# Kernel optimization log

Hardware: AMD Instinct MI355X
Metric: run time of the kernel (lower is better)

The kernel has to match this reference:

```python
import jax, jax.numpy as jnp
import numpy as np
import math

B, S, HID, H, WBAND = 2, 4096, 768, 12, 128
D = HID // H  # 64


def _band_qk(q, k, w):
    """q,k: [B,S,H,D] -> banded scores [B,S,H,2w+1] (offset d -> key pos i+d-w)."""
    b, s, h, d = q.shape
    nc = s // w
    kp = jnp.pad(k, ((0, 0), (w, w), (0, 0), (0, 0)))  # zero padding_value
    idx = (jnp.arange(nc) * w)[:, None] + jnp.arange(3 * w)[None, :]  # [nc,3w]
    kw = kp[:, idx]                                   # [B,nc,3w,H,D]
    qc = q.reshape(b, nc, w, h, d)
    scores = jnp.einsum('bcxhd,bcyhd->bchxy', qc, kw)  # [B,nc,H,w,3w]
    # extract diagonals: P[x,dd] = scores[x, x+dd] via flatten/skew trick
    flat = scores.reshape(b, nc, h, w * 3 * w)
    flat = jnp.pad(flat, ((0, 0), (0, 0), (0, 0), (0, w)))
    diag = flat.reshape(b, nc, h, w, 3 * w + 1)[..., : 2 * w + 1]
    return diag.transpose(0, 1, 3, 2, 4).reshape(b, s, h, 2 * w + 1)


def _band_pv(p, v, w):
    """p: [B,S,H,2w+1], v: [B,S,H,D] -> context [B,S,H,D]."""
    b, s, h, k = p.shape
    d = v.shape[-1]
    nc = s // w
    vp = jnp.pad(v, ((0, 0), (w, w), (0, 0), (0, 0)))
    idx = (jnp.arange(nc) * w)[:, None] + jnp.arange(3 * w)[None, :]
    vw = vp[:, idx]                                   # [B,nc,3w,H,D]
    pc = p.reshape(b, nc, w, h, k).transpose(0, 1, 3, 2, 4)  # [B,nc,H,w,2w+1]
    pc = jnp.pad(pc, ((0, 0), (0, 0), (0, 0), (0, 0), (0, w)))  # [..,w,3w+1]
    band = pc.reshape(b, nc, h, w * (3 * w + 1))[..., : w * 3 * w]
    band = band.reshape(b, nc, h, w, 3 * w)           # M[x, x+dd] = p[x,dd]
    ctx = jnp.einsum('bchxy,bcyhd->bcxhd', band, vw)  # [B,nc,w,H,D]
    return ctx.reshape(b, s, h, d)


def setup_inputs() -> dict:
    key = jax.random.key(0)
    ks = jax.random.split(key, 8)
    init = lambda k, shp: (jax.random.normal(k, shp, jnp.float32) * 0.02)
    return {
        'x': jax.random.normal(ks[0], (B, S, HID), jnp.float32),
        'Wq': init(ks[1], (HID, HID)), 'bq': jnp.zeros((HID,), jnp.float32),
        'Wk': init(ks[2], (HID, HID)), 'bk': jnp.zeros((HID,), jnp.float32),
        'Wv': init(ks[3], (HID, HID)), 'bv': jnp.zeros((HID,), jnp.float32),
        'Wd': init(ks[4], (H, D, HID)), 'bd': jnp.zeros((HID,), jnp.float32),
        'gamma': jnp.ones((HID,), jnp.float32),
        'beta': jnp.zeros((HID,), jnp.float32),
    }


def reference(x, Wq, bq, Wk, bk, Wv, bv, Wd, bd, gamma, beta):
    w = WBAND
    b, s, _ = x.shape
    q = (x @ Wq + bq).reshape(b, s, H, D) / math.sqrt(D)
    k = (x @ Wk + bk).reshape(b, s, H, D)
    v = (x @ Wv + bv).reshape(b, s, H, D)
    scores = _band_qk(q, k, w)                        # [B,S,H,2w+1]
    # mask_invalid_locations: key pos i + d - w must lie in [0, S)
    pos = jnp.arange(s)[:, None] + jnp.arange(2 * w + 1)[None, :] - w
    valid = (pos >= 0) & (pos < s)                    # [S,2w+1]
    scores = jnp.where(valid[None, :, None, :], scores, -1e9)
    probs = jax.nn.softmax(scores, axis=-1)           # float32 softmax
    ctx = _band_pv(probs, v, w)                       # [B,S,H,D]
    proj = jnp.einsum('bfnd,ndh->bfh', ctx, Wd) + bd  # output projection
    y = x + proj                                      # residual (dropout=0)
    mu = jnp.mean(y, axis=-1, keepdims=True)
    var = jnp.mean(jnp.square(y - mu), axis=-1, keepdims=True)
    out = (y - mu) / jnp.sqrt(var + 1e-12) * gamma + beta
    return out
```

## Files before the change

### kernel.cpp

```cpp
#include <hip/hip_runtime.h>
#include <math.h>

typedef unsigned short u16;
typedef __bf16 bf16x8 __attribute__((ext_vector_type(8)));
typedef float f32x4 __attribute__((ext_vector_type(4)));

constexpr int Bc   = 2;
constexpr int Sc   = 4096;
constexpr int HIDc = 768;
constexpr int Hc   = 12;
constexpr int Dc   = 64;
constexpr int Wc   = 128;
constexpr int Mc   = Bc * Sc;

constexpr int QT3  = 128;
constexpr int NCT3 = 18;

#define VM_BAR(N) asm volatile("s_waitcnt vmcnt(" #N ")\n\ts_barrier" ::: "memory")
#define BAR()     asm volatile("s_barrier" ::: "memory")

static __device__ __forceinline__ void load_lds16(const void* g, void* l) {
    __builtin_amdgcn_global_load_lds(
        (const __attribute__((address_space(1))) void*)g,
        (__attribute__((address_space(3))) void*)l, 16, 0, 0);
}
static __device__ __forceinline__ u16 to_bf16(float f) {
    return __builtin_bit_cast(u16, (__bf16)f);
}

__global__ __launch_bounds__(256) void prep_all(
    const float* __restrict__ x, u16* __restrict__ xb, u16* __restrict__ zpad,
    const float* __restrict__ Wq, const float* __restrict__ Wk,
    const float* __restrict__ Wv, const float* __restrict__ Wd,
    u16* __restrict__ wqt, u16* __restrict__ wkt,
    u16* __restrict__ wvt, u16* __restrict__ wdt)
{
    const int bid = blockIdx.x;
    if (bid < 6144) {
        int i = bid * 256 + threadIdx.x;
        float4 v = ((const float4*)x)[i];
        ushort4 o;
        o.x = to_bf16(v.x); o.y = to_bf16(v.y);
        o.z = to_bf16(v.z); o.w = to_bf16(v.w);
        ((ushort4*)xb)[i] = o;
        if (bid == 0 && threadIdx.x < 128)
            ((int4*)zpad)[threadIdx.x] = make_int4(0, 0, 0, 0);
    } else {
        int r = bid - 6144;
        int z = r / 576, xy = r - z * 576;
        const float* W = z == 0 ? Wq : z == 1 ? Wk : z == 2 ? Wv : Wd;
        u16* T         = z == 0 ? wqt : z == 1 ? wkt : z == 2 ? wvt : wdt;
        __shared__ float t[32][33];
        const int bx = (xy % 24) * 32, by = (xy / 24) * 32;
        const int tx = threadIdx.x & 31, ty = threadIdx.x >> 5;
#pragma unroll
        for (int i = 0; i < 32; i += 8)
            t[ty + i][tx] = W[(size_t)(by + ty + i) * HIDc + bx + tx];
        __syncthreads();
#pragma unroll
        for (int i = 0; i < 32; i += 8)
            T[(size_t)(bx + ty + i) * HIDc + by + tx] = to_bf16(t[tx][ty + i]);
    }
}

__device__ __forceinline__ void stage64(const u16* __restrict__ A,
                                        const u16* __restrict__ Bt,
                                        int m0, int n0, int k0,
                                        u16* As, u16* Bs, int soff)
{
#pragma unroll
    for (int i = 0; i < 4; ++i) {
        int off  = soff + i * 1024;
        int row  = off >> 7;
        int slot = (off >> 4) & 7;
        int seg  = slot ^ (row & 7);
        load_lds16(A  + (size_t)(m0 + row) * HIDc + k0 + seg * 8, (char*)As + off);
        load_lds16(Bt + (size_t)(n0 + row) * HIDc + k0 + seg * 8, (char*)Bs + off);
    }
}

template <int SWAP>
__device__ __forceinline__ void gemm128_core(
    const u16* __restrict__ A, const u16* __restrict__ Bt,
    int m0, int n0, u16* As, u16* Bs, f32x4 (&acc)[4][4])
{
    const int lane = threadIdx.x & 63, wid = threadIdx.x >> 6;
    const int c16 = lane & 15, g = lane >> 4;
    const int wm = (wid >> 1) * 64, wn = (wid & 1) * 64;
    const int soff = wid * 4096 + lane * 16;

    stage64(A, Bt, m0, n0, 0, As, Bs, soff);
    int cur = 0;
    for (int t = 0; t < 12; ++t) {
        if (t < 11) {
            stage64(A, Bt, m0, n0, (t + 1) * 64,
                    As + (cur ^ 1) * 8192, Bs + (cur ^ 1) * 8192, soff);
            VM_BAR(8);
        } else {
            VM_BAR(0);
        }
        const u16* Ab = As + cur * 8192;
        const u16* Bb = Bs + cur * 8192;
#pragma unroll
        for (int kk = 0; kk < 2; ++kk) {
            bf16x8 af[4], bfr[4];
#pragma unroll
            for (int tt = 0; tt < 4; ++tt) {
                int ar = wm + tt * 16 + c16;
                int a8 = (kk * 4 + g) ^ (ar & 7);
                af[tt] = *(const bf16x8*)(Ab + ar * 64 + a8 * 8);
                int br = wn + tt * 16 + c16;
                int b8 = (kk * 4 + g) ^ (br & 7);
                bfr[tt] = *(const bf16x8*)(Bb + br * 64 + b8 * 8);
            }
            __builtin_amdgcn_s_setprio(1);
#pragma unroll
            for (int mt = 0; mt < 4; ++mt)
#pragma unroll
                for (int nt = 0; nt < 4; ++nt)
                    acc[mt][nt] = SWAP
                        ? __builtin_amdgcn_mfma_f32_16x16x32_bf16(
                              bfr[nt], af[mt], acc[mt][nt], 0, 0, 0)
                        : __builtin_amdgcn_mfma_f32_16x16x32_bf16(
                              af[mt], bfr[nt], acc[mt][nt], 0, 0, 0);
            __builtin_amdgcn_s_setprio(0);
        }
        BAR();
        cur ^= 1;
    }
}

__global__ __launch_bounds__(256) void gemm_qkv_mfma(
    const u16* __restrict__ xb,
    const u16* __restrict__ wqt, const u16* __restrict__ wkt,
    const u16* __restrict__ wvt,
    const float* __restrict__ bq, const float* __restrict__ bk,
    const float* __restrict__ bv,
    u16* __restrict__ qg, u16* __restrict__ kg, u16* __restrict__ vtg)
{
    __shared__ u16 As[16384], Bs[16384];
    const int z = blockIdx.z;
    const u16* Bt     = z == 0 ? wqt : z == 1 ? wkt : wvt;
    const float* bias = z == 0 ? bq : z == 1 ? bk : bv;

    const int m0 = blockIdx.x * 128, n0 = blockIdx.y * 128;
    f32x4 acc[4][4];
#pragma unroll
    for (int i = 0; i < 4; ++i)
#pragma unroll
        for (int j = 0; j < 4; ++j) acc[i][j] = (f32x4){0.f, 0.f, 0.f, 0.f};

    const int lane = threadIdx.x & 63, wid = threadIdx.x >> 6;
    const int c16 = lane & 15, g = lane >> 4;
    const int wm = (wid >> 1) * 64, wn = (wid & 1) * 64;

    if (z == 2) {
        gemm128_core<0>(xb, Bt, m0, n0, As, Bs, acc);
#pragma unroll
        for (int nt = 0; nt < 4; ++nt) {
            int n = n0 + wn + nt * 16 + c16;
            int h = n >> 6, d = n & 63;
            float bn = bias[n];
#pragma unroll
            for (int mt = 0; mt < 4; ++mt) {
                int m = m0 + wm + mt * 16 + g * 4;
                int b = m >> 12, s = m & (Sc - 1);
                size_t base = ((size_t)(b * Hc + h)) * Sc * Dc + (size_t)d * Sc + s;
                ushort4 pk;
                pk.x = to_bf16(acc[mt][nt][0] + bn);
                pk.y = to_bf16(acc[mt][nt][1] + bn);
                pk.z = to_bf16(acc[mt][nt][2] + bn);
                pk.w = to_bf16(acc[mt][nt][3] + bn);
                *(ushort4*)&vtg[base] = pk;
            }
        }
    } else {
        gemm128_core<1>(xb, Bt, m0, n0, As, Bs, acc);
        const float scale = z ? 1.0f : 0.125f;
        u16* outp = z ? kg : qg;
#pragma unroll
        for (int mt = 0; mt < 4; ++mt) {
            int m = m0 + wm + mt * 16 + c16;
            int b = m >> 12, s = m & (Sc - 1);
            size_t rowbase = (size_t)(b * Hc) * Sc * Dc + (size_t)s * Dc;
#pragma unroll
            for (int nt = 0; nt < 4; ++nt) {
                int nb = n0 + wn + nt * 16 + g * 4;
                int h = nb >> 6, d0 = nb & 63;
                float4 b4 = *(const float4*)&bias[nb];
                ushort4 pk;
                pk.x = to_bf16((acc[mt][nt][0] + b4.x) * scale);
                pk.y = to_bf16((acc[mt][nt][1] + b4.y) * scale);
                pk.z = to_bf16((acc[mt][nt][2] + b4.z) * scale);
                pk.w = to_bf16((acc[mt][nt][3] + b4.w) * scale);
                *(ushort4*)&outp[rowbase + (size_t)h * Sc * Dc + d0] = pk;
            }
        }
    }
}

__global__ __launch_bounds__(256) void gemm_proj_mfma(
    const u16* __restrict__ ctxb, const u16* __restrict__ wdt,
    const float* __restrict__ bd, const float* __restrict__ x,
    float* __restrict__ y)
{
    __shared__ u16 As[16384], Bs[16384];
    const int m0 = blockIdx.x * 128, n0 = blockIdx.y * 128;
    f32x4 acc[4][4];
#pragma unroll
    for (int i = 0; i < 4; ++i)
#pragma unroll
        for (int j = 0; j < 4; ++j) acc[i][j] = (f32x4){0.f, 0.f, 0.f, 0.f};

    gemm128_core<1>(ctxb, wdt, m0, n0, As, Bs, acc);

    const int lane = threadIdx.x & 63, wid = threadIdx.x >> 6;
    const int c16 = lane & 15, g = lane >> 4;
    const int wm = (wid >> 1) * 64, wn = (wid & 1) * 64;

#pragma unroll
    for (int mt = 0; mt < 4; ++mt) {
        int m = m0 + wm + mt * 16 + c16;
#pragma unroll
        for (int nt = 0; nt < 4; ++nt) {
            int nb = n0 + wn + nt * 16 + g * 4;
            float4 b4 = *(const float4*)&bd[nb];
            float4 x4 = *(const float4*)&x[(size_t)m * HIDc + nb];
            float4 o4;
            o4.x = acc[mt][nt][0] + b4.x + x4.x;
            o4.y = acc[mt][nt][1] + b4.y + x4.y;
            o4.z = acc[mt][nt][2] + b4.z + x4.z;
            o4.w = acc[mt][nt][3] + b4.w + x4.w;
            *(float4*)&y[(size_t)m * HIDc + nb] = o4;
        }
    }
}

__global__ __launch_bounds__(512) void band_attn_mfma(
    const u16* __restrict__ qg, const u16* __restrict__ kg,
    const u16* __restrict__ vtg, const u16* __restrict__ zpad,
    u16* __restrict__ ctxb)
{
    extern __shared__ u16 sm[];
    u16* kwin = sm;
    u16* vt   = sm + 24576;
    u16* pm   = sm;

    const int L = blockIdx.x;
    const int xcd = L & 7, tt = L >> 3;
    const int hb = xcd * 3 + (tt % 3);
    const int qc = tt / 3;
    const int h = hb % Hc, b = hb / Hc;

    const int s0 = qc * QT3;
    const int tid = threadIdx.x;
    const int lane = tid & 63, w = tid >> 6;
    const int c16 = lane & 15, g = lane >> 4;
    const size_t hbase = ((size_t)(b * Hc + h)) * Sc * Dc;

    const u16* qp = &qg[hbase + (size_t)(s0 + w * 16 + c16) * Dc + g * 8];
    bf16x8 qa0 = *(const bf16x8*)qp;
    bf16x8 qa1 = *(const bf16x8*)(qp + 32);

#pragma unroll
    for (int i = 0; i < 6; ++i) {
        int c   = i * 8 + w;
        int row = c * 8 + (lane >> 3);
        int seg = (lane & 7) ^ (lane >> 3);
        int pos = s0 - Wc + row;
        const u16* src = (pos >= 0 && pos < Sc)
                       ? &kg[hbase + (size_t)pos * Dc + seg * 8] : zpad;
        load_lds16(src, (char*)kwin + c * 1024 + (lane & 63) * 16);
    }
#pragma unroll
    for (int i = 0; i < 6; ++i) {
        int c   = i * 8 + w;
        int idx = c * 64 + lane;
        int d   = idx / 48;
        int p   = idx - d * 48;
        int seg = (p & ~7) | ((p ^ d) & 7);
        int pos0 = s0 - Wc + seg * 8;
        const u16* src = (pos0 >= 0 && pos0 < Sc)
                       ? &vtg[hbase + (size_t)d * Sc + pos0] : zpad;
        load_lds16(src, (char*)vt + idx * 16);
    }

    VM_BAR(6);

    const int tb  = w & ~1;
    const int off = (w & 1) * 16;
    f32x4 acc[NCT3];
#pragma unroll
    for (int ct = 0; ct < NCT3; ++ct) acc[ct] = (f32x4){0.f, 0.f, 0.f, 0.f};
    __builtin_amdgcn_s_setprio(1);
#pragma unroll
    for (int ct = 0; ct < NCT3; ++ct) {
        int row = (tb + ct) * 16 + c16;
        const u16* kb = kwin + row * 64;
        bf16x8 kb0 = *(const bf16x8*)(kb + (g       ^ (row & 7)) * 8);
        bf16x8 kb1 = *(const bf16x8*)(kb + ((g + 4) ^ (row & 7)) * 8);
        acc[ct] = __builtin_amdgcn_mfma_f32_16x16x32_bf16(qa0, kb0, acc[ct], 0, 0, 0);
        acc[ct] = __builtin_amdgcn_mfma_f32_16x16x32_bf16(qa1, kb1, acc[ct], 0, 0, 0);
    }
    __builtin_amdgcn_s_setprio(0);

    float mrow[4] = {-3e38f, -3e38f, -3e38f, -3e38f};
#pragma unroll
    for (int ct = 0; ct < NCT3; ++ct) {
#pragma unroll
        for (int r = 0; r < 4; ++r) {
            int ql  = g * 4 + r;
            int jl  = ct * 16 + c16 - off;
            int pos = s0 - Wc + (tb + ct) * 16 + c16;
            bool valid = (jl >= ql) && (jl <= ql + 2 * Wc) && (pos >= 0) && (pos < Sc);
            float v = valid ? acc[ct][r] : -3e38f;
            acc[ct][r] = v;
            mrow[r] = fmaxf(mrow[r], v);
        }
    }
#pragma unroll
    for (int r = 0; r < 4; ++r)
#pragma unroll
        for (int o2 = 1; o2 < 16; o2 <<= 1)
            mrow[r] = fmaxf(mrow[r], __shfl_xor(mrow[r], o2));

    float srow[4] = {0.f, 0.f, 0.f, 0.f};
#pragma unroll
    for (int ct = 0; ct < NCT3; ++ct)
#pragma unroll
        for (int r = 0; r < 4; ++r) {
            float e = __expf(acc[ct][r] - mrow[r]);
            acc[ct][r] = e;
            srow[r] += e;
        }
#pragma unroll
    for (int r = 0; r < 4; ++r)
#pragma unroll
        for (int o2 = 1; o2 < 16; o2 <<= 1)
            srow[r] += __shfl_xor(srow[r], o2);

    VM_BAR(0);

    float sq0 = __shfl(srow[0], (c16 >> 2) << 4);
    float sq1 = __shfl(srow[1], (c16 >> 2) << 4);
    float sq2 = __shfl(srow[2], (c16 >> 2) << 4);
    float sq3 = __shfl(srow[3], (c16 >> 2) << 4);
    int rr = c16 & 3;
    float sq = rr == 0 ? sq0 : rr == 1 ? sq1 : rr == 2 ? sq2 : sq3;
    float invq = 1.f / sq;

    const int qrow = w * 16 + c16;
    f32x4 o[4];
#pragma unroll
    for (int dt = 0; dt < 4; ++dt) o[dt] = (f32x4){0.f, 0.f, 0.f, 0.f};

#pragma unroll
    for (int ct = 0; ct < 10; ++ct)
#pragma unroll
        for (int r = 0; r < 4; ++r) {
            int q   = w * 16 + g * 4 + r;
            int col = ct * 16 + c16;
            int sl  = col >> 3;
            int ph  = (sl & ~7) | ((sl ^ q ^ (q >> 3)) & 7);
            pm[q * 192 + ph * 8 + (col & 7)] = to_bf16(acc[ct][r]);
        }
    __builtin_amdgcn_s_setprio(1);
#pragma unroll
    for (int ks = 0; ks < 5; ++ks) {
        int sl = ks * 4 + g;
        int ph = (sl & ~7) | ((sl ^ qrow ^ (qrow >> 3)) & 7);
        bf16x8 pa = *(const bf16x8*)(pm + qrow * 192 + ph * 8);
#pragma unroll
        for (int dt = 0; dt < 4; ++dt) {
            int d  = dt * 16 + c16;
            int vs = tb * 2 + ks * 4 + g;
            int pv = (vs & ~7) | ((vs ^ d) & 7);
            bf16x8 vb = *(const bf16x8*)(vt + d * 384 + pv * 8);
            o[dt] = __builtin_amdgcn_mfma_f32_16x16x32_bf16(vb, pa, o[dt], 0, 0, 0);
        }
    }
    __builtin_amdgcn_s_setprio(0);

#pragma unroll
    for (int ct = 10; ct < NCT3; ++ct)
#pragma unroll
        for (int r = 0; r < 4; ++r) {
            int q   = w * 16 + g * 4 + r;
            int col = ct * 16 + c16 - 160;
            int sl  = col >> 3;
            int ph  = (sl & ~7) | ((sl ^ q ^ (q >> 3)) & 7);
            pm[q * 192 + ph * 8 + (col & 7)] = to_bf16(acc[ct][r]);
        }
    __builtin_amdgcn_s_setprio(1);
#pragma unroll
    for (int ks = 0; ks < 4; ++ks) {
        int sl = ks * 4 + g;
        int ph = (sl & ~7) | ((sl ^ qrow ^ (qrow >> 3)) & 7);
        bf16x8 pa = *(const bf16x8*)(pm + qrow * 192 + ph * 8);
#pragma unroll
        for (int dt = 0; dt < 4; ++dt) {
            int d  = dt * 16 + c16;
            int vs = tb * 2 + 20 + ks * 4 + g;
            int pv = (vs & ~7) | ((vs ^ d) & 7);
            bf16x8 vb = *(const bf16x8*)(vt + d * 384 + pv * 8);
            o[dt] = __builtin_amdgcn_mfma_f32_16x16x32_bf16(vb, pa, o[dt], 0, 0, 0);
        }
    }
    __builtin_amdgcn_s_setprio(0);

    const size_t crow = ((size_t)(b * Sc + s0 + qrow)) * HIDc + h * Dc;
#pragma unroll
    for (int dt = 0; dt < 4; ++dt) {
        ushort4 pk;
        pk.x = to_bf16(o[dt][0] * invq);
        pk.y = to_bf16(o[dt][1] * invq);
        pk.z = to_bf16(o[dt][2] * invq);
        pk.w = to_bf16(o[dt][3] * invq);
        *(ushort4*)&ctxb[crow + dt * 16 + g * 4] = pk;
    }
}

__global__ __launch_bounds__(256) void ln_kernel(
    const float* __restrict__ y,
    const float* __restrict__ gamma, const float* __restrict__ beta,
    float* __restrict__ out)
{
    const int m = blockIdx.x;
    const float* row = y + (size_t)m * HIDc;
    const int t = threadIdx.x;
    float v0 = row[t], v1 = row[t + 256], v2 = row[t + 512];
    float s = v0 + v1 + v2;
    __shared__ float red[4];
    const int lane = t & 63, wid = t >> 6;
#pragma unroll
    for (int o = 1; o < 64; o <<= 1) s += __shfl_xor(s, o);
    if (lane == 0) red[wid] = s;
    __syncthreads();
    const float mu = (red[0] + red[1] + red[2] + red[3]) * (1.f / HIDc);
    v0 -= mu; v1 -= mu; v2 -= mu;
    float s2 = v0 * v0 + v1 * v1 + v2 * v2;
#pragma unroll
    for (int o = 1; o < 64; o <<= 1) s2 += __shfl_xor(s2, o);
    __syncthreads();
    if (lane == 0) red[wid] = s2;
    __syncthreads();
    const float var = (red[0] + red[1] + red[2] + red[3]) * (1.f / HIDc);
    const float rstd = rsqrtf(var + 1e-12f);
    const size_t base = (size_t)m * HIDc;
    out[base + t]       = v0 * rstd * gamma[t]       + beta[t];
    out[base + t + 256] = v1 * rstd * gamma[t + 256] + beta[t + 256];
    out[base + t + 512] = v2 * rstd * gamma[t + 512] + beta[t + 512];
}

extern "C" void kernel_launch(void* const* d_in, const int* in_sizes, int n_in,
                              void* d_out, int out_size, void* d_ws, size_t ws_size,
                              hipStream_t stream)
{
    const float* x     = (const float*)d_in[0];
    const float* Wq    = (const float*)d_in[1];
    const float* bq    = (const float*)d_in[2];
    const float* Wk    = (const float*)d_in[3];
    const float* bk    = (const float*)d_in[4];
    const float* Wv    = (const float*)d_in[5];
    const float* bv    = (const float*)d_in[6];
    const float* Wd    = (const float*)d_in[7];
    const float* bd    = (const float*)d_in[8];
    const float* gamma = (const float*)d_in[9];
    const float* beta  = (const float*)d_in[10];
    float* out = (float*)d_out;

    constexpr size_t CHUNK = (size_t)Mc * HIDc;
    constexpr size_t WSZ   = (size_t)HIDc * HIDc;
    u16* xb   = (u16*)d_ws;
    u16* wqt  = xb + CHUNK;
    u16* wkt  = wqt + WSZ;
    u16* wvt  = wkt + WSZ;
    u16* wdt  = wvt + WSZ;
    u16* qg   = wdt + WSZ;
    u16* kg   = qg + CHUNK;
    u16* vtg  = kg + CHUNK;
    u16* ctxb = vtg + CHUNK;
    float* yws = (float*)(ctxb + CHUNK);
    u16* zpad  = (u16*)(yws + CHUNK);

    prep_all<<<6144 + 2304, 256, 0, stream>>>(
        x, xb, zpad, Wq, Wk, Wv, Wd, wqt, wkt, wvt, wdt);

    gemm_qkv_mfma<<<dim3(Mc / 128, HIDc / 128, 3), 256, 0, stream>>>(
        xb, wqt, wkt, wvt, bq, bk, bv, qg, kg, vtg);

    band_attn_mfma<<<dim3(Sc / QT3 * Hc * Bc), 512, 98304, stream>>>(
        qg, kg, vtg, zpad, ctxb);

    gemm_proj_mfma<<<dim3(Mc / 128, HIDc / 128), 256, 0, stream>>>(
        ctxb, wdt, bd, x, yws);

    ln_kernel<<<Mc, 256, 0, stream>>>(yws, gamma, beta, out);
}
```

Baseline: 123.6 us.

## Enlarge GEMM tiles to 256x128 with 8 waves and triple-buffered LDS

The QKV and output-projection GEMMs now use 512-thread blocks computing 256x128 tiles, so each B tile loaded into LDS is shared by twice as many rows. The double-buffered K pipeline becomes triple-buffered, prefetching two k-steps ahead with adjusted vmcnt waits, and shared memory moves to dynamic allocation (144 KB). The aim is less global traffic per FLOP and better hiding of load latency. The cost is half as many blocks in the grid and lower occupancy from the large LDS footprint.

```diff
diff --git a/kernel.cpp b/kernel.cpp
--- a/kernel.cpp
+++ b/kernel.cpp
@@ -63,44 +63,58 @@
     }
 }
 
-__device__ __forceinline__ void stage64(const u16* __restrict__ A,
-                                        const u16* __restrict__ Bt,
-                                        int m0, int n0, int k0,
-                                        u16* As, u16* Bs, int soff)
-{
+__device__ __forceinline__ void stageA(const u16* __restrict__ A,
+                                       int m0, int k0, u16* lds)
+{
+    const int tid = threadIdx.x;
 #pragma unroll
     for (int i = 0; i < 4; ++i) {
-        int off  = soff + i * 1024;
+        int off  = tid * 16 + i * 8192;
         int row  = off >> 7;
         int slot = (off >> 4) & 7;
         int seg  = slot ^ (row & 7);
-        load_lds16(A  + (size_t)(m0 + row) * HIDc + k0 + seg * 8, (char*)As + off);
-        load_lds16(Bt + (size_t)(n0 + row) * HIDc + k0 + seg * 8, (char*)Bs + off);
+        load_lds16(A + (size_t)(m0 + row) * HIDc + k0 + seg * 8, (char*)lds + off);
+    }
+}
+__device__ __forceinline__ void stageB(const u16* __restrict__ Bt,
+                                       int n0, int k0, u16* lds)
+{
+    const int tid = threadIdx.x;
+#pragma unroll
+    for (int i = 0; i < 2; ++i) {
+        int off  = tid * 16 + i * 8192;
+        int row  = off >> 7;
+        int slot = (off >> 4) & 7;
+        int seg  = slot ^ (row & 7);
+        load_lds16(Bt + (size_t)(n0 + row) * HIDc + k0 + seg * 8, (char*)lds + off);
     }
 }
 
 template <int SWAP>
-__device__ __forceinline__ void gemm128_core(
+__device__ __forceinline__ void gemm256_core(
     const u16* __restrict__ A, const u16* __restrict__ Bt,
     int m0, int n0, u16* As, u16* Bs, f32x4 (&acc)[4][4])
 {
-    const int lane = threadIdx.x & 63, wid = threadIdx.x >> 6;
+    const int lane = threadIdx.x & 63, w = threadIdx.x >> 6;
     const int c16 = lane & 15, g = lane >> 4;
-    const int wm = (wid >> 1) * 64, wn = (wid & 1) * 64;
-    const int soff = wid * 4096 + lane * 16;
-
-    stage64(A, Bt, m0, n0, 0, As, Bs, soff);
-    int cur = 0;
+    const int wm = (w >> 1) * 64, wn = (w & 1) * 64;
+
+    stageA(A, m0, 0, As);          stageB(Bt, n0, 0, Bs);
+    stageA(A, m0, 64, As + 16384); stageB(Bt, n0, 64, Bs + 8192);
+
+    int cb = 0, sb = 2;
     for (int t = 0; t < 12; ++t) {
-        if (t < 11) {
-            stage64(A, Bt, m0, n0, (t + 1) * 64,
-                    As + (cur ^ 1) * 8192, Bs + (cur ^ 1) * 8192, soff);
-            VM_BAR(8);
+        if (t < 10) {
+            stageA(A, m0, (t + 2) * 64, As + sb * 16384);
+            stageB(Bt, n0, (t + 2) * 64, Bs + sb * 8192);
+            VM_BAR(12);
+        } else if (t == 10) {
+            VM_BAR(6);
         } else {
             VM_BAR(0);
         }
-        const u16* Ab = As + cur * 8192;
-        const u16* Bb = Bs + cur * 8192;
+        const u16* Ab = As + cb * 16384;
+        const u16* Bb = Bs + cb * 8192;
 #pragma unroll
         for (int kk = 0; kk < 2; ++kk) {
             bf16x8 af[4], bfr[4];
@@ -126,11 +140,12 @@
             __builtin_amdgcn_s_setprio(0);
         }
         BAR();
-        cur ^= 1;
-    }
-}
-
-__global__ __launch_bounds__(256) void gemm_qkv_mfma(
+        cb = cb == 2 ? 0 : cb + 1;
+        sb = sb == 2 ? 0 : sb + 1;
+    }
+}
+
+__global__ __launch_bounds__(512) void gemm_qkv_mfma(
     const u16* __restrict__ xb,
     const u16* __restrict__ wqt, const u16* __restrict__ wkt,
     const u16* __restrict__ wvt,
@@ -138,24 +153,27 @@
     const float* __restrict__ bv,
     u16* __restrict__ qg, u16* __restrict__ kg, u16* __restrict__ vtg)
 {
-    __shared__ u16 As[16384], Bs[16384];
+    extern __shared__ u16 smg[];
+    u16* As = smg;
+    u16* Bs = smg + 3 * 16384;
+
     const int z = blockIdx.z;
     const u16* Bt     = z == 0 ? wqt : z == 1 ? wkt : wvt;
     const float* bias = z == 0 ? bq : z == 1 ? bk : bv;
 
-    const int m0 = blockIdx.x * 128, n0 = blockIdx.y * 128;
+    const int m0 = blockIdx.x * 256, n0 = blockIdx.y * 128;
     f32x4 acc[4][4];
 #pragma unroll
     for (int i = 0; i < 4; ++i)
 #pragma unroll
         for (int j = 0; j < 4; ++j) acc[i][j] = (f32x4){0.f, 0.f, 0.f, 0.f};
 
-    const int lane = threadIdx.x & 63, wid = threadIdx.x >> 6;
+    const int lane = threadIdx.x & 63, w = threadIdx.x >> 6;
     const int c16 = lane & 15, g = lane >> 4;
-    const int wm = (wid >> 1) * 64, wn = (wid & 1) * 64;
+    const int wm = (w >> 1) * 64, wn = (w & 1) * 64;
 
     if (z == 2) {
-        gemm128_core<0>(xb, Bt, m0, n0, As, Bs, acc);
+        gemm256_core<0>(xb, Bt, m0, n0, As, Bs, acc);
 #pragma unroll
         for (int nt = 0; nt < 4; ++nt) {
             int n = n0 + wn + nt * 16 + c16;
@@ -175,7 +193,7 @@
             }
         }
     } else {
-        gemm128_core<1>(xb, Bt, m0, n0, As, Bs, acc);
+        gemm256_core<1>(xb, Bt, m0, n0, As, Bs, acc);
         const float scale = z ? 1.0f : 0.125f;
         u16* outp = z ? kg : qg;
 #pragma unroll
@@ -199,24 +217,27 @@
     }
 }
 
-__global__ __launch_bounds__(256) void gemm_proj_mfma(
+__global__ __launch_bounds__(512) void gemm_proj_mfma(
     const u16* __restrict__ ctxb, const u16* __restrict__ wdt,
     const float* __restrict__ bd, const float* __restrict__ x,
     float* __restrict__ y)
 {
-    __shared__ u16 As[16384], Bs[16384];
-    const int m0 = blockIdx.x * 128, n0 = blockIdx.y * 128;
+    extern __shared__ u16 smg[];
+    u16* As = smg;
+    u16* Bs = smg + 3 * 16384;
+
+    const int m0 = blockIdx.x * 256, n0 = blockIdx.y * 128;
     f32x4 acc[4][4];
 #pragma unroll
     for (int i = 0; i < 4; ++i)
 #pragma unroll
         for (int j = 0; j < 4; ++j) acc[i][j] = (f32x4){0.f, 0.f, 0.f, 0.f};
 
-    gemm128_core<1>(ctxb, wdt, m0, n0, As, Bs, acc);
-
-    const int lane = threadIdx.x & 63, wid = threadIdx.x >> 6;
+    gemm256_core<1>(ctxb, wdt, m0, n0, As, Bs, acc);
+
+    const int lane = threadIdx.x & 63, w = threadIdx.x >> 6;
     const int c16 = lane & 15, g = lane >> 4;
-    const int wm = (wid >> 1) * 64, wn = (wid & 1) * 64;
+    const int wm = (w >> 1) * 64, wn = (w & 1) * 64;
 
 #pragma unroll
     for (int mt = 0; mt < 4; ++mt) {
@@ -483,16 +504,18 @@
     float* yws = (float*)(ctxb + CHUNK);
     u16* zpad  = (u16*)(yws + CHUNK);
 
+    constexpr size_t GEMM_LDS = (3 * 16384 + 3 * 8192) * sizeof(u16);
+
     prep_all<<<6144 + 2304, 256, 0, stream>>>(
         x, xb, zpad, Wq, Wk, Wv, Wd, wqt, wkt, wvt, wdt);
 
-    gemm_qkv_mfma<<<dim3(Mc / 128, HIDc / 128, 3), 256, 0, stream>>>(
+    gemm_qkv_mfma<<<dim3(Mc / 256, HIDc / 128, 3), 512, GEMM_LDS, stream>>>(
         xb, wqt, wkt, wvt, bq, bk, bv, qg, kg, vtg);
 
     band_attn_mfma<<<dim3(Sc / QT3 * Hc * Bc), 512, 98304, stream>>>(
         qg, kg, vtg, zpad, ctxb);
 
-    gemm_proj_mfma<<<dim3(Mc / 128, HIDc / 128), 256, 0, stream>>>(
+    gemm_proj_mfma<<<dim3(Mc / 256, HIDc / 128), 512, GEMM_LDS, stream>>>(
         ctxb, wdt, bd, x, yws);
 
     ln_kernel<<<Mc, 256, 0, stream>>>(yws, gamma, beta, out);
```

Result: slower. 128.8 us (+4.2%).

## Load GEMM weight fragments directly from global memory, staging only A in LDS

Applied to the files above, without the earlier changes.

The shared GEMM core no longer stages the weight (B) tile through LDS. Each wave now reads its B fragments straight from global memory into registers, while A alone goes through the double-buffered LDS path. This halves LDS use per block, which could allow higher occupancy, and removes the LDS write/read traffic for B. In exchange, the B register loads are issued right before use with little latency hiding and are read redundantly by the two waves sharing a column tile, relying on cache hits.

```diff
diff --git a/kernel.cpp b/kernel.cpp
--- a/kernel.cpp
+++ b/kernel.cpp
@@ -63,55 +63,56 @@
     }
 }
 
-__device__ __forceinline__ void stage64(const u16* __restrict__ A,
-                                        const u16* __restrict__ Bt,
-                                        int m0, int n0, int k0,
-                                        u16* As, u16* Bs, int soff)
-{
+__device__ __forceinline__ void stageA64(const u16* __restrict__ A,
+                                         int m0, int k0, u16* lds)
+{
+    const int tid = threadIdx.x;
 #pragma unroll
     for (int i = 0; i < 4; ++i) {
-        int off  = soff + i * 1024;
+        int off  = tid * 16 + i * 4096;
         int row  = off >> 7;
         int slot = (off >> 4) & 7;
         int seg  = slot ^ (row & 7);
-        load_lds16(A  + (size_t)(m0 + row) * HIDc + k0 + seg * 8, (char*)As + off);
-        load_lds16(Bt + (size_t)(n0 + row) * HIDc + k0 + seg * 8, (char*)Bs + off);
+        load_lds16(A + (size_t)(m0 + row) * HIDc + k0 + seg * 8, (char*)lds + off);
     }
 }
 
 template <int SWAP>
-__device__ __forceinline__ void gemm128_core(
+__device__ __forceinline__ void gemm128_bdir(
     const u16* __restrict__ A, const u16* __restrict__ Bt,
-    int m0, int n0, u16* As, u16* Bs, f32x4 (&acc)[4][4])
+    int m0, int n0, u16* As, f32x4 (&acc)[4][4])
 {
     const int lane = threadIdx.x & 63, wid = threadIdx.x >> 6;
     const int c16 = lane & 15, g = lane >> 4;
     const int wm = (wid >> 1) * 64, wn = (wid & 1) * 64;
-    const int soff = wid * 4096 + lane * 16;
-
-    stage64(A, Bt, m0, n0, 0, As, Bs, soff);
+
+    const u16* bbase = Bt + (size_t)(n0 + wn + c16) * HIDc + g * 8;
+
+    stageA64(A, m0, 0, As);
     int cur = 0;
     for (int t = 0; t < 12; ++t) {
+        bf16x8 bf0[4], bf1[4];
+        const u16* bt = bbase + t * 64;
+#pragma unroll
+        for (int tt = 0; tt < 4; ++tt) {
+            bf0[tt] = *(const bf16x8*)(bt + (size_t)tt * 16 * HIDc);
+            bf1[tt] = *(const bf16x8*)(bt + (size_t)tt * 16 * HIDc + 32);
+        }
         if (t < 11) {
-            stage64(A, Bt, m0, n0, (t + 1) * 64,
-                    As + (cur ^ 1) * 8192, Bs + (cur ^ 1) * 8192, soff);
-            VM_BAR(8);
+            stageA64(A, m0, (t + 1) * 64, As + (cur ^ 1) * 8192);
+            VM_BAR(4);
         } else {
             VM_BAR(0);
         }
         const u16* Ab = As + cur * 8192;
-        const u16* Bb = Bs + cur * 8192;
 #pragma unroll
         for (int kk = 0; kk < 2; ++kk) {
-            bf16x8 af[4], bfr[4];
+            bf16x8 af[4];
 #pragma unroll
             for (int tt = 0; tt < 4; ++tt) {
                 int ar = wm + tt * 16 + c16;
                 int a8 = (kk * 4 + g) ^ (ar & 7);
                 af[tt] = *(const bf16x8*)(Ab + ar * 64 + a8 * 8);
-                int br = wn + tt * 16 + c16;
-                int b8 = (kk * 4 + g) ^ (br & 7);
-                bfr[tt] = *(const bf16x8*)(Bb + br * 64 + b8 * 8);
             }
             __builtin_amdgcn_s_setprio(1);
 #pragma unroll
@@ -120,9 +121,9 @@
                 for (int nt = 0; nt < 4; ++nt)
                     acc[mt][nt] = SWAP
                         ? __builtin_amdgcn_mfma_f32_16x16x32_bf16(
-                              bfr[nt], af[mt], acc[mt][nt], 0, 0, 0)
+                              kk ? bf1[nt] : bf0[nt], af[mt], acc[mt][nt], 0, 0, 0)
                         : __builtin_amdgcn_mfma_f32_16x16x32_bf16(
-                              af[mt], bfr[nt], acc[mt][nt], 0, 0, 0);
+                              af[mt], kk ? bf1[nt] : bf0[nt], acc[mt][nt], 0, 0, 0);
             __builtin_amdgcn_s_setprio(0);
         }
         BAR();
@@ -138,7 +139,7 @@
     const float* __restrict__ bv,
     u16* __restrict__ qg, u16* __restrict__ kg, u16* __restrict__ vtg)
 {
-    __shared__ u16 As[16384], Bs[16384];
+    __shared__ u16 As[16384];
     const int z = blockIdx.z;
     const u16* Bt     = z == 0 ? wqt : z == 1 ? wkt : wvt;
     const float* bias = z == 0 ? bq : z == 1 ? bk : bv;
@@ -155,7 +156,7 @@
     const int wm = (wid >> 1) * 64, wn = (wid & 1) * 64;
 
     if (z == 2) {
-        gemm128_core<0>(xb, Bt, m0, n0, As, Bs, acc);
+        gemm128_bdir<0>(xb, Bt, m0, n0, As, acc);
 #pragma unroll
         for (int nt = 0; nt < 4; ++nt) {
             int n = n0 + wn + nt * 16 + c16;
@@ -175,7 +176,7 @@
             }
         }
     } else {
-        gemm128_core<1>(xb, Bt, m0, n0, As, Bs, acc);
+        gemm128_bdir<1>(xb, Bt, m0, n0, As, acc);
         const float scale = z ? 1.0f : 0.125f;
         u16* outp = z ? kg : qg;
 #pragma unroll
@@ -204,7 +205,7 @@
     const float* __restrict__ bd, const float* __restrict__ x,
     float* __restrict__ y)
 {
-    __shared__ u16 As[16384], Bs[16384];
+    __shared__ u16 As[16384];
     const int m0 = blockIdx.x * 128, n0 = blockIdx.y * 128;
     f32x4 acc[4][4];
 #pragma unroll
@@ -212,7 +213,7 @@
 #pragma unroll
         for (int j = 0; j < 4; ++j) acc[i][j] = (f32x4){0.f, 0.f, 0.f, 0.f};
 
-    gemm128_core<1>(ctxb, wdt, m0, n0, As, Bs, acc);
+    gemm128_bdir<1>(ctxb, wdt, m0, n0, As, acc);
 
     const int lane = threadIdx.x & 63, wid = threadIdx.x >> 6;
     const int c16 = lane & 15, g = lane >> 4;
```

After: 165.3 us. 1.34x slower.

## Load K and V directly from global memory instead of staging in LDS

Applied to the files above, without the earlier changes.

Drops the cooperative global-to-LDS staging of the K window and transposed V window. Each wave now reads its K and V fragments straight from global memory into registers, and only the probability matrix stays in a smaller static shared array. This removes the LDS copy and its barriers and halves shared memory use so more blocks can fit per CU, with a min-blocks launch bound added. The cost is redundant global/cache traffic across waves and less coalesced access. K rows outside the sequence are now read unguarded from adjacent memory and rely on the later mask.

```diff
diff --git a/kernel.cpp b/kernel.cpp
--- a/kernel.cpp
+++ b/kernel.cpp
@@ -236,15 +236,12 @@
     }
 }
 
-__global__ __launch_bounds__(512) void band_attn_mfma(
+__global__ __launch_bounds__(512, 4) void band_attn_mfma(
     const u16* __restrict__ qg, const u16* __restrict__ kg,
     const u16* __restrict__ vtg, const u16* __restrict__ zpad,
     u16* __restrict__ ctxb)
 {
-    extern __shared__ u16 sm[];
-    u16* kwin = sm;
-    u16* vt   = sm + 24576;
-    u16* pm   = sm;
+    __shared__ u16 pm[128 * 192];
 
     const int L = blockIdx.x;
     const int xcd = L & 7, tt = L >> 3;
@@ -262,43 +259,19 @@
     bf16x8 qa0 = *(const bf16x8*)qp;
     bf16x8 qa1 = *(const bf16x8*)(qp + 32);
 
-#pragma unroll
-    for (int i = 0; i < 6; ++i) {
-        int c   = i * 8 + w;
-        int row = c * 8 + (lane >> 3);
-        int seg = (lane & 7) ^ (lane >> 3);
-        int pos = s0 - Wc + row;
-        const u16* src = (pos >= 0 && pos < Sc)
-                       ? &kg[hbase + (size_t)pos * Dc + seg * 8] : zpad;
-        load_lds16(src, (char*)kwin + c * 1024 + (lane & 63) * 16);
-    }
-#pragma unroll
-    for (int i = 0; i < 6; ++i) {
-        int c   = i * 8 + w;
-        int idx = c * 64 + lane;
-        int d   = idx / 48;
-        int p   = idx - d * 48;
-        int seg = (p & ~7) | ((p ^ d) & 7);
-        int pos0 = s0 - Wc + seg * 8;
-        const u16* src = (pos0 >= 0 && pos0 < Sc)
-                       ? &vtg[hbase + (size_t)d * Sc + pos0] : zpad;
-        load_lds16(src, (char*)vt + idx * 16);
-    }
-
-    VM_BAR(6);
-
     const int tb  = w & ~1;
     const int off = (w & 1) * 16;
+
     f32x4 acc[NCT3];
 #pragma unroll
     for (int ct = 0; ct < NCT3; ++ct) acc[ct] = (f32x4){0.f, 0.f, 0.f, 0.f};
     __builtin_amdgcn_s_setprio(1);
 #pragma unroll
     for (int ct = 0; ct < NCT3; ++ct) {
-        int row = (tb + ct) * 16 + c16;
-        const u16* kb = kwin + row * 64;
-        bf16x8 kb0 = *(const bf16x8*)(kb + (g       ^ (row & 7)) * 8);
-        bf16x8 kb1 = *(const bf16x8*)(kb + ((g + 4) ^ (row & 7)) * 8);
+        int pos = s0 - Wc + (tb + ct) * 16 + c16;
+        const u16* kp = kg + hbase + (size_t)pos * Dc + g * 8;
+        bf16x8 kb0 = *(const bf16x8*)kp;
+        bf16x8 kb1 = *(const bf16x8*)(kp + 32);
         acc[ct] = __builtin_amdgcn_mfma_f32_16x16x32_bf16(qa0, kb0, acc[ct], 0, 0, 0);
         acc[ct] = __builtin_amdgcn_mfma_f32_16x16x32_bf16(qa1, kb1, acc[ct], 0, 0, 0);
     }
@@ -339,8 +312,6 @@
         for (int o2 = 1; o2 < 16; o2 <<= 1)
             srow[r] += __shfl_xor(srow[r], o2);
 
-    VM_BAR(0);
-
     float sq0 = __shfl(srow[0], (c16 >> 2) << 4);
     float sq1 = __shfl(srow[1], (c16 >> 2) << 4);
     float sq2 = __shfl(srow[2], (c16 >> 2) << 4);
@@ -370,12 +341,14 @@
         int sl = ks * 4 + g;
         int ph = (sl & ~7) | ((sl ^ qrow ^ (qrow >> 3)) & 7);
         bf16x8 pa = *(const bf16x8*)(pm + qrow * 192 + ph * 8);
+        int vs   = tb * 2 + sl;
+        int pos0 = s0 - Wc + vs * 8;
+        bool ok  = (pos0 >= 0) && (pos0 <= Sc - 8);
 #pragma unroll
         for (int dt = 0; dt < 4; ++dt) {
-            int d  = dt * 16 + c16;
-            int vs = tb * 2 + ks * 4 + g;
-            int pv = (vs & ~7) | ((vs ^ d) & 7);
-            bf16x8 vb = *(const bf16x8*)(vt + d * 384 + pv * 8);
+            int d = dt * 16 + c16;
+            const u16* vp = ok ? (vtg + hbase + (size_t)d * Sc + pos0) : zpad;
+            bf16x8 vb = *(const bf16x8*)vp;
             o[dt] = __builtin_amdgcn_mfma_f32_16x16x32_bf16(vb, pa, o[dt], 0, 0, 0);
         }
     }
@@ -397,12 +370,14 @@
         int sl = ks * 4 + g;
         int ph = (sl & ~7) | ((sl ^ qrow ^ (qrow >> 3)) & 7);
         bf16x8 pa = *(const bf16x8*)(pm + qrow * 192 + ph * 8);
+        int vs   = tb * 2 + 20 + sl;
+        int pos0 = s0 - Wc + vs * 8;
+        bool ok  = (pos0 >= 0) && (pos0 <= Sc - 8);
 #pragma unroll
         for (int dt = 0; dt < 4; ++dt) {
-            int d  = dt * 16 + c16;
-            int vs = tb * 2 + 20 + ks * 4 + g;
-            int pv = (vs & ~7) | ((vs ^ d) & 7);
-            bf16x8 vb = *(const bf16x8*)(vt + d * 384 + pv * 8);
+            int d = dt * 16 + c16;
+            const u16* vp = ok ? (vtg + hbase + (size_t)d * Sc + pos0) : zpad;
+            bf16x8 vb = *(const bf16x8*)vp;
             o[dt] = __builtin_amdgcn_mfma_f32_16x16x32_bf16(vb, pa, o[dt], 0, 0, 0);
         }
     }
@@ -489,7 +464,7 @@
     gemm_qkv_mfma<<<dim3(Mc / 128, HIDc / 128, 3), 256, 0, stream>>>(
         xb, wqt, wkt, wvt, bq, bk, bv, qg, kg, vtg);
 
-    band_attn_mfma<<<dim3(Sc / QT3 * Hc * Bc), 512, 98304, stream>>>(
+    band_attn_mfma<<<dim3(Sc / QT3 * Hc * Bc), 512, 0, stream>>>(
         qg, kg, vtg, zpad, ctxb);
 
     gemm_proj_mfma<<<dim3(Mc / 128, HIDc / 128), 256, 0, stream>>>(
```

New measurement: 158.7 us. 28.4% more time.
